# Kernel optimization log

Hardware: AMD Instinct MI355X
Metric: run time of the kernel (lower is better)

The kernel has to match this reference:

```python
import jax, jax.numpy as jnp
import numpy as np

N, D, K = 8192, 512, 256


def setup_inputs() -> dict:
    key = jax.random.key(0)
    k1, k2, k3 = jax.random.split(key, 3)
    features = jax.random.normal(k1, (N, D), dtype=jnp.float32)
    adjacency = jax.random.uniform(k2, (N, N), dtype=jnp.float32)
    W = jax.random.normal(k3, (D, K), dtype=jnp.float32) / np.sqrt(D)
    b = jnp.zeros((K,), dtype=jnp.float32)
    return {"features": features, "adjacency": adjacency, "W": W, "b": b}


def reference(features, adjacency, W, b):
    # logits = Linear(features): (n, k)
    logits = features @ W + b
    # activation == 'softmax' (torch F.softmax on 2D defaults to dim=1)
    assignments = jax.nn.softmax(logits, axis=-1)            # (n, k)
    cluster_sizes = jnp.sum(assignments, axis=0)             # (k,)
    sp = assignments / (cluster_sizes + 1e-8)                # normalized assignments (n, k)
    features_pooled = sp.T @ features                        # (k, d)
    adjacency_pooled = (sp.T @ adjacency) @ sp               # (k, k) -- computed in original forward
    # link loss: ||A - S S^T||_F / numel(A)
    diff = adjacency - sp @ sp.T                             # (n, n)
    link_loss = jnp.sqrt(jnp.sum(diff * diff)) / adjacency.size
    # entropy loss on normalized assignments
    ent_loss = jnp.mean(jnp.sum(-sp * jnp.log(sp + 1e-15), axis=-1))
    return features_pooled, assignments, adjacency_pooled, link_loss, ent_loss
```

## Files before the change

kernel.cpp:

```cpp
#include <hip/hip_runtime.h>


typedef unsigned short u16;
typedef __bf16 bf16x8 __attribute__((ext_vector_type(8)));
typedef float f32x4 __attribute__((ext_vector_type(4)));
typedef float float8_t __attribute__((ext_vector_type(8)));
typedef unsigned short ushort8_t __attribute__((ext_vector_type(8)));

#define Nn 8192
#define Dd 512
#define Kk 256

__device__ __forceinline__ u16 f2bf(float f) {
  unsigned int u = __builtin_bit_cast(unsigned int, f);
  u += 0x7FFFu + ((u >> 16) & 1u);
  return (u16)(u >> 16);
}
__device__ __forceinline__ float bf2f(u16 h) {
  return __builtin_bit_cast(float, (unsigned int)h << 16);
}
__device__ __forceinline__ void gll16(const void* g, void* l) {
  __builtin_amdgcn_global_load_lds(
      (const __attribute__((address_space(1))) unsigned int*)g,
      (__attribute__((address_space(3))) unsigned int*)l, 16, 0, 0);
}

template <bool SUMSQ, int OUTKIND, int OCC>
__launch_bounds__(256, OCC)
__global__ void gemm2(const u16* __restrict__ Apan, int ppmb,
                      const float* __restrict__ Bv, int ldb,
                      void* __restrict__ Cv, int ldc,
                      int kchunk, size_t zstride,
                      float* __restrict__ sumsq, int swz) {
  __shared__ alignas(16) u16 SH[2 * 8192 + 2 * 2048];
  float* sred = (float*)&SH[20472];

  int bx = blockIdx.x, bz = blockIdx.z;
  if (swz) {
    int gx = gridDim.x, tot = gx * gridDim.z;
    int f = bx + gx * bz;
    int l = (f & 7) * (tot >> 3) + (f >> 3);
    bx = l % gx; bz = l / gx;
  }
  const int tid = threadIdx.x, wv = tid >> 6, lane = tid & 63;
  const int l15 = lane & 15, g = lane >> 4;
  const int col0 = bx * 64;
  const int row0 = blockIdx.y * 256;
  const int kbeg = bz * kchunk;
  const int steps = kchunk >> 5;
  const u16* pbase = Apan + (size_t)(blockIdx.y * ppmb + (kbeg >> 5)) * 8192;

  float ss = 0.f;
  float8_t rb;

  auto loadB = [&](int t) {
    const int kq = kbeg + t * 32 + wv * 8;
    const float* p = Bv + (size_t)kq * ldb + col0 + lane;
#pragma unroll
    for (int i = 0; i < 8; ++i) rb[i] = p[(size_t)i * ldb];
  };
  auto storeB = [&](int buf) {
    ushort8_t h;
#pragma unroll
    for (int i = 0; i < 8; ++i) {
      h[i] = f2bf(rb[i]);
      if constexpr (SUMSQ) ss += rb[i] * rb[i];
    }
    *(uint4*)&SH[16384 + buf * 2048 + lane * 32 + wv * 8] = __builtin_bit_cast(uint4, h);
  };
  auto gllA = [&](int buf, int t) {
    const char* gp = (const char*)(pbase + (size_t)t * 8192) + wv * 4096 + lane * 16;
    char* lp = (char*)&SH[buf * 8192] + wv * 4096;
#pragma unroll
    for (int r = 0; r < 4; ++r) gll16(gp + r * 1024, lp + r * 1024);
  };

  f32x4 acc[4][4];
#pragma unroll
  for (int i = 0; i < 4; ++i)
#pragma unroll
    for (int j = 0; j < 4; ++j) acc[i][j] = (f32x4){0.f, 0.f, 0.f, 0.f};

  auto comp = [&](int buf) {
    const u16* as = &SH[buf * 8192];
    const u16* bs = &SH[16384 + buf * 2048];
    bf16x8 afr[4], bfr[4];
#pragma unroll
    for (int j = 0; j < 4; ++j)
      bfr[j] = *(const bf16x8*)(bs + (j * 16 + l15) * 32 + g * 8);
#pragma unroll
    for (int i = 0; i < 4; ++i)
      afr[i] = *(const bf16x8*)(as + (wv * 64 + i * 16 + l15) * 32 + g * 8);
#pragma unroll
    for (int i = 0; i < 4; ++i)
#pragma unroll
      for (int j = 0; j < 4; ++j)
        acc[i][j] = __builtin_amdgcn_mfma_f32_16x16x32_bf16(afr[i], bfr[j], acc[i][j], 0, 0, 0);
  };

  gllA(0, 0);
  loadB(0);
  const int last = steps - 1;

  for (int t = 0; t < steps; ++t) {
    const int cur = t & 1;
    gllA(1 - cur, (t + 1 < last) ? t + 1 : last);
    storeB(cur);
    loadB((t + 1 < last) ? t + 1 : last);
    asm volatile("s_waitcnt vmcnt(12) lgkmcnt(0)" ::: "memory");
    __builtin_amdgcn_s_barrier();
    __builtin_amdgcn_sched_barrier(0);
    comp(cur);
    __builtin_amdgcn_sched_barrier(0);
    __builtin_amdgcn_s_barrier();
  }
  asm volatile("s_waitcnt vmcnt(0) lgkmcnt(0)" ::: "memory");
  __builtin_amdgcn_s_barrier();

  if constexpr (OUTKIND == 0) {
    float* Cz = (float*)Cv + (size_t)bz * zstride;
    float* sf = (float*)SH;
#pragma unroll
    for (int h = 0; h < 2; ++h) {
      __syncthreads();
      if ((wv >> 1) == h) {
#pragma unroll
        for (int i = 0; i < 4; ++i)
#pragma unroll
          for (int j = 0; j < 4; ++j)
#pragma unroll
            for (int r = 0; r < 4; ++r)
              sf[((wv & 1) * 64 + i * 16 + g * 4 + r) * 68 + j * 16 + l15] = acc[i][j][r];
      }
      __syncthreads();
#pragma unroll
      for (int e = 0; e < 8; ++e) {
        int idx2 = tid + e * 256;
        int m = idx2 >> 4, c4 = (idx2 & 15) * 4;
        float4 v = *(const float4*)(sf + m * 68 + c4);
        *(float4*)(Cz + (size_t)(row0 + h * 128 + m) * ldc + col0 + c4) = v;
      }
    }
  } else {
    u16* C = (u16*)Cv + (size_t)bz * zstride;
    u16* sb = SH;
#pragma unroll
    for (int i = 0; i < 4; ++i)
#pragma unroll
      for (int j = 0; j < 4; ++j)
#pragma unroll
        for (int r = 0; r < 4; ++r)
          sb[(wv * 64 + i * 16 + g * 4 + r) * 72 + j * 16 + l15] = f2bf(acc[i][j][r]);
    __syncthreads();
#pragma unroll
    for (int e = 0; e < 8; ++e) {
      int m = (tid >> 3) + e * 32;
      uint4 v = *(const uint4*)(sb + m * 72 + (tid & 7) * 8);
      *(uint4*)(C + (size_t)m * ldc + col0 + (tid & 7) * 8) = v;
    }
  }

  if constexpr (SUMSQ) {
#pragma unroll
    for (int o = 32; o; o >>= 1) ss += __shfl_xor(ss, o);
    __syncthreads();
    if (lane == 0) sred[wv] = ss;
    __syncthreads();
    if (tid == 0) atomicAdd(sumsq, sred[0] + sred[1] + sred[2] + sred[3]);
  }
}

__launch_bounds__(256, 2)
__global__ void gemm1(const float* __restrict__ F, const float* __restrict__ W,
                      float* __restrict__ Cv, size_t zstride) {
  __shared__ alignas(16) u16 SH[2 * 8192 + 2 * 2048];

  const int tid = threadIdx.x, wv = tid >> 6, lane = tid & 63;
  const int l15 = lane & 15, g = lane >> 4;
  const int col0 = blockIdx.x * 64;
  const int row0 = blockIdx.y * 256;
  const int kbeg = blockIdx.z * 256;
  const int mrow = tid >> 3, kq4 = (tid & 7) * 4;

  float4 rA[8];
  float8_t rb;

  auto loadA = [&](int t) {
    const float* p = F + (size_t)(row0 + mrow) * Dd + kbeg + t * 32 + kq4;
#pragma unroll
    for (int i = 0; i < 8; ++i) rA[i] = *(const float4*)(p + (size_t)i * 32 * Dd);
  };
  auto storeA = [&](int buf) {
    u16* as = &SH[buf * 8192];
#pragma unroll
    for (int i = 0; i < 8; ++i) {
      ushort4 h = {f2bf(rA[i].x), f2bf(rA[i].y), f2bf(rA[i].z), f2bf(rA[i].w)};
      *(uint2*)(as + (mrow + i * 32) * 32 + kq4) = __builtin_bit_cast(uint2, h);
    }
  };
  auto loadB = [&](int t) {
    const int kq = kbeg + t * 32 + wv * 8;
    const float* p = W + (size_t)kq * Kk + col0 + lane;
#pragma unroll
    for (int i = 0; i < 8; ++i) rb[i] = p[(size_t)i * Kk];
  };
  auto storeB = [&](int buf) {
    ushort8_t h;
#pragma unroll
    for (int i = 0; i < 8; ++i) h[i] = f2bf(rb[i]);
    *(uint4*)&SH[16384 + buf * 2048 + lane * 32 + wv * 8] = __builtin_bit_cast(uint4, h);
  };

  f32x4 acc[4][4];
#pragma unroll
  for (int i = 0; i < 4; ++i)
#pragma unroll
    for (int j = 0; j < 4; ++j) acc[i][j] = (f32x4){0.f, 0.f, 0.f, 0.f};

  auto comp = [&](int buf) {
    const u16* as = &SH[buf * 8192];
    const u16* bs = &SH[16384 + buf * 2048];
    bf16x8 afr[4], bfr[4];
#pragma unroll
    for (int j = 0; j < 4; ++j)
      bfr[j] = *(const bf16x8*)(bs + (j * 16 + l15) * 32 + g * 8);
#pragma unroll
    for (int i = 0; i < 4; ++i)
      afr[i] = *(const bf16x8*)(as + (wv * 64 + i * 16 + l15) * 32 + g * 8);
#pragma unroll
    for (int i = 0; i < 4; ++i)
#pragma unroll
      for (int j = 0; j < 4; ++j)
        acc[i][j] = __builtin_amdgcn_mfma_f32_16x16x32_bf16(afr[i], bfr[j], acc[i][j], 0, 0, 0);
  };

  loadA(0);
  loadB(0);
  for (int t = 0; t < 8; ++t) {
    const int cur = t & 1;
    storeA(cur);
    storeB(cur);
    loadA((t + 1 < 8) ? t + 1 : 7);
    loadB((t + 1 < 8) ? t + 1 : 7);
    asm volatile("s_waitcnt vmcnt(16) lgkmcnt(0)" ::: "memory");
    __builtin_amdgcn_s_barrier();
    __builtin_amdgcn_sched_barrier(0);
    comp(cur);
    __builtin_amdgcn_sched_barrier(0);
    __builtin_amdgcn_s_barrier();
  }
  asm volatile("s_waitcnt vmcnt(0) lgkmcnt(0)" ::: "memory");
  __builtin_amdgcn_s_barrier();

  float* Cz = Cv + (size_t)blockIdx.z * zstride;
  float* sf = (float*)SH;
#pragma unroll
  for (int h = 0; h < 2; ++h) {
    __syncthreads();
    if ((wv >> 1) == h) {
#pragma unroll
      for (int i = 0; i < 4; ++i)
#pragma unroll
        for (int j = 0; j < 4; ++j)
#pragma unroll
          for (int r = 0; r < 4; ++r)
            sf[((wv & 1) * 64 + i * 16 + g * 4 + r) * 68 + j * 16 + l15] = acc[i][j][r];
    }
    __syncthreads();
#pragma unroll
    for (int e = 0; e < 8; ++e) {
      int idx2 = tid + e * 256;
      int m = idx2 >> 4, c4 = (idx2 & 15) * 4;
      float4 v = *(const float4*)(sf + m * 68 + c4);
      *(float4*)(Cz + (size_t)(row0 + h * 128 + m) * Kk + col0 + c4) = v;
    }
  }
}

__launch_bounds__(256, 2)
__global__ void gemm45(const u16* __restrict__ spTpan,
                       const float* __restrict__ F, float* __restrict__ fp_part,
                       const float* __restrict__ assign, float* __restrict__ ss_part) {
  __shared__ alignas(16) u16 SH[2 * 8192 + 2 * 2048];

  const int b = blockIdx.x;
  int bx, bz, ldb, ldc;
  const float* Bf;
  float* Cz;
  if (b < 256) {
    bx = b & 7; bz = b >> 3;
    Bf = F; ldb = Dd; ldc = Dd;
    Cz = fp_part + (size_t)bz * 131072;
  } else {
    int lb = b - 256;
    bx = lb & 3; bz = lb >> 2;
    Bf = assign; ldb = Kk; ldc = Kk;
    Cz = ss_part + (size_t)bz * 65536;
  }
  const int tid = threadIdx.x, wv = tid >> 6, lane = tid & 63;
  const int l15 = lane & 15, g = lane >> 4;
  const int col0 = bx * 64;
  const int kbeg = bz * 256;
  const u16* pbase = spTpan + (size_t)(kbeg >> 5) * 8192;

  float8_t rb;
  auto loadB = [&](int t) {
    const int kq = kbeg + t * 32 + wv * 8;
    const float* p = Bf + (size_t)kq * ldb + col0 + lane;
#pragma unroll
    for (int i = 0; i < 8; ++i) rb[i] = p[(size_t)i * ldb];
  };
  auto storeB = [&](int buf) {
    ushort8_t h;
#pragma unroll
    for (int i = 0; i < 8; ++i) h[i] = f2bf(rb[i]);
    *(uint4*)&SH[16384 + buf * 2048 + lane * 32 + wv * 8] = __builtin_bit_cast(uint4, h);
  };
  auto gllA = [&](int buf, int t) {
    const char* gp = (const char*)(pbase + (size_t)t * 8192) + wv * 4096 + lane * 16;
    char* lp = (char*)&SH[buf * 8192] + wv * 4096;
#pragma unroll
    for (int r = 0; r < 4; ++r) gll16(gp + r * 1024, lp + r * 1024);
  };

  f32x4 acc[4][4];
#pragma unroll
  for (int i = 0; i < 4; ++i)
#pragma unroll
    for (int j = 0; j < 4; ++j) acc[i][j] = (f32x4){0.f, 0.f, 0.f, 0.f};

  auto comp = [&](int buf) {
    const u16* as = &SH[buf * 8192];
    const u16* bs = &SH[16384 + buf * 2048];
    bf16x8 afr[4], bfr[4];
#pragma unroll
    for (int j = 0; j < 4; ++j)
      bfr[j] = *(const bf16x8*)(bs + (j * 16 + l15) * 32 + g * 8);
#pragma unroll
    for (int i = 0; i < 4; ++i)
      afr[i] = *(const bf16x8*)(as + (wv * 64 + i * 16 + l15) * 32 + g * 8);
#pragma unroll
    for (int i = 0; i < 4; ++i)
#pragma unroll
      for (int j = 0; j < 4; ++j)
        acc[i][j] = __builtin_amdgcn_mfma_f32_16x16x32_bf16(afr[i], bfr[j], acc[i][j], 0, 0, 0);
  };

  gllA(0, 0);
  loadB(0);
  const int last = 7;
  for (int t = 0; t < 8; ++t) {
    const int cur = t & 1;
    gllA(1 - cur, (t + 1 < last) ? t + 1 : last);
    storeB(cur);
    loadB((t + 1 < last) ? t + 1 : last);
    asm volatile("s_waitcnt vmcnt(12) lgkmcnt(0)" ::: "memory");
    __builtin_amdgcn_s_barrier();
    __builtin_amdgcn_sched_barrier(0);
    comp(cur);
    __builtin_amdgcn_sched_barrier(0);
    __builtin_amdgcn_s_barrier();
  }
  asm volatile("s_waitcnt vmcnt(0) lgkmcnt(0)" ::: "memory");
  __builtin_amdgcn_s_barrier();

  float* sf = (float*)SH;
#pragma unroll
  for (int h = 0; h < 2; ++h) {
    __syncthreads();
    if ((wv >> 1) == h) {
#pragma unroll
      for (int i = 0; i < 4; ++i)
#pragma unroll
        for (int j = 0; j < 4; ++j)
#pragma unroll
          for (int r = 0; r < 4; ++r)
            sf[((wv & 1) * 64 + i * 16 + g * 4 + r) * 68 + j * 16 + l15] = acc[i][j][r];
    }
    __syncthreads();
#pragma unroll
    for (int e = 0; e < 8; ++e) {
      int idx2 = tid + e * 256;
      int m = idx2 >> 4, c4 = (idx2 & 15) * 4;
      float4 v = *(const float4*)(sf + m * 68 + c4);
      *(float4*)(Cz + (size_t)(h * 128 + m) * ldc + col0 + c4) = v;
    }
  }
}

__launch_bounds__(256)
__global__ void softmax_rows(const float* __restrict__ lg, float* __restrict__ io,
                             const float* __restrict__ bias,
                             float* __restrict__ cs, float* __restrict__ scal) {
  if (blockIdx.x == 2048) {
    int t = threadIdx.x;
    float4 z = {0.f, 0.f, 0.f, 0.f};
    if (t < 64) ((float4*)cs)[t] = z;
    else if (t == 64) ((float4*)scal)[0] = z;
    return;
  }
  int wv = threadIdx.x >> 6, lane = threadIdx.x & 63;
  int n = blockIdx.x * 4 + wv;
  float4 b4 = ((const float4*)bias)[lane];
  float4 p0 = ((const float4*)(lg + (size_t)n * Kk))[lane];
  float4 p1 = ((const float4*)(lg + 2097152 + (size_t)n * Kk))[lane];
  float4 x = {p0.x + p1.x + b4.x, p0.y + p1.y + b4.y,
              p0.z + p1.z + b4.z, p0.w + p1.w + b4.w};
  float m = fmaxf(fmaxf(x.x, x.y), fmaxf(x.z, x.w));
#pragma unroll
  for (int o = 32; o; o >>= 1) m = fmaxf(m, __shfl_xor(m, o));
  float4 e = {__expf(x.x - m), __expf(x.y - m), __expf(x.z - m), __expf(x.w - m)};
  float s = e.x + e.y + e.z + e.w;
#pragma unroll
  for (int o = 32; o; o >>= 1) s += __shfl_xor(s, o);
  float inv = 1.f / s;
  e.x *= inv; e.y *= inv; e.z *= inv; e.w *= inv;
  ((float4*)(io + (size_t)n * Kk))[lane] = e;
}

__launch_bounds__(256)
__global__ void colsum_k(const float* __restrict__ a, float* __restrict__ cs) {
  __shared__ float4 red[4][64];
  int t = threadIdx.x, rg = t >> 6, c = t & 63;
  size_t n0 = (size_t)blockIdx.x * 128 + rg * 32;
  float4 s = {0.f, 0.f, 0.f, 0.f};
  for (int i = 0; i < 32; ++i) {
    float4 v = ((const float4*)(a + (n0 + i) * Kk))[c];
    s.x += v.x; s.y += v.y; s.z += v.z; s.w += v.w;
  }
  red[rg][c] = s;
  __syncthreads();
  if (rg == 0) {
    float4 a1 = red[1][c], a2 = red[2][c], a3 = red[3][c];
    s.x += a1.x + a2.x + a3.x; s.y += a1.y + a2.y + a3.y;
    s.z += a1.z + a2.z + a3.z; s.w += a1.w + a2.w + a3.w;
    atomicAdd(&cs[c * 4 + 0], s.x); atomicAdd(&cs[c * 4 + 1], s.y);
    atomicAdd(&cs[c * 4 + 2], s.z); atomicAdd(&cs[c * 4 + 3], s.w);
  }
}

__launch_bounds__(256)
__global__ void make_sp_pan(const float* __restrict__ a, const float* __restrict__ cs,
                            u16* __restrict__ pan, float* __restrict__ ent_sum) {
  __shared__ float sr[4];
  int p = blockIdx.x, k = threadIdx.x;
  float inv = 1.f / (cs[k] + 1e-8f);
  int n0 = p * 32;
  float ent = 0.f;
  ushort8_t h[4];
#pragma unroll
  for (int q = 0; q < 4; ++q) {
#pragma unroll
    for (int j = 0; j < 8; ++j) {
      float v = a[(size_t)(n0 + q * 8 + j) * Kk + k] * inv;
      h[q][j] = f2bf(v);
      ent -= v * __logf(v + 1e-15f);
    }
  }
  u16* dst = pan + ((size_t)p * 256 + k) * 32;
  *(uint4*)(dst + 0)  = __builtin_bit_cast(uint4, h[0]);
  *(uint4*)(dst + 8)  = __builtin_bit_cast(uint4, h[1]);
  *(uint4*)(dst + 16) = __builtin_bit_cast(uint4, h[2]);
  *(uint4*)(dst + 24) = __builtin_bit_cast(uint4, h[3]);
#pragma unroll
  for (int o = 32; o; o >>= 1) ent += __shfl_xor(ent, o);
  if ((k & 63) == 0) sr[k >> 6] = ent;
  __syncthreads();
  if (k == 0) atomicAdd(ent_sum, sr[0] + sr[1] + sr[2] + sr[3]);
}

__launch_bounds__(256)
__global__ void combine_P(const u16* __restrict__ part, u16* __restrict__ pan) {
  int idx = blockIdx.x * 256 + threadIdx.x;
  int m = idx >> 10, kk8 = idx & 1023;
  size_t off = (size_t)m * Nn + kk8 * 8;
  float8_t s = {0.f, 0.f, 0.f, 0.f, 0.f, 0.f, 0.f, 0.f};
#pragma unroll
  for (int z = 0; z < 8; ++z) {
    ushort8_t v = __builtin_bit_cast(ushort8_t,
        *(const uint4*)(part + (size_t)z * Kk * Nn + off));
#pragma unroll
    for (int j = 0; j < 8; ++j) s[j] += bf2f(v[j]);
  }
  ushort8_t h;
#pragma unroll
  for (int j = 0; j < 8; ++j) h[j] = f2bf(s[j]);
  int p = kk8 >> 2, c = (kk8 & 3) * 8;
  *(uint4*)(pan + ((size_t)p * 256 + m) * 32 + c) = __builtin_bit_cast(uint4, h);
}

__launch_bounds__(256)
__global__ void combine3(const float* __restrict__ fp_part, const float* __restrict__ ss_part,
                         const float* __restrict__ ap_part, const float* __restrict__ cs,
                         float* __restrict__ fpool, float* __restrict__ apool,
                         float* __restrict__ scal) {
  __shared__ float sr[4];
  int b = blockIdx.x, t = threadIdx.x;
  if (b < 512) {
    int i = b * 256 + t;
    float s = 0.f;
#pragma unroll
    for (int z = 0; z < 32; ++z) s += fp_part[z * 131072 + i];
    fpool[i] = s;
  } else if (b < 768) {
    int i = (b - 512) * 256 + t;
    float s = 0.f;
#pragma unroll
    for (int z = 0; z < 32; ++z) s += ss_part[z * 65536 + i];
    s *= 1.f / (cs[i & 255] + 1e-8f);
    float q = s * s;
#pragma unroll
    for (int o = 32; o; o >>= 1) q += __shfl_xor(q, o);
    if ((t & 63) == 0) sr[t >> 6] = q;
    __syncthreads();
    if (t == 0) atomicAdd(&scal[2], sr[0] + sr[1] + sr[2] + sr[3]);
  } else {
    int i = (b - 768) * 256 + t;
    float s = 0.f;
#pragma unroll
    for (int z = 0; z < 32; ++z) s += ap_part[z * 65536 + i];
    s *= 1.f / (cs[i & 255] + 1e-8f);
    apool[i] = s;
    if (i % 257 == 0) atomicAdd(&scal[3], s);
  }
}

__launch_bounds__(64)
__global__ void finalize_k(const float* __restrict__ scal,
                           float* __restrict__ olink, float* __restrict__ oent) {
  if (threadIdx.x == 0) {
    float val = scal[0] - 2.f * scal[3] + scal[2];
    *olink = sqrtf(fmaxf(val, 0.f)) / ((float)Nn * (float)Nn);
    *oent  = scal[1] / (float)Nn;
  }
}

extern "C" void kernel_launch(void* const* d_in, const int* in_sizes, int n_in,
                              void* d_out, int out_size, void* d_ws, size_t ws_size,
                              hipStream_t stream) {
  const float* F    = (const float*)d_in[0];
  const float* Adj  = (const float*)d_in[1];
  const float* W    = (const float*)d_in[2];
  const float* bias = (const float*)d_in[3];
  float* out = (float*)d_out;
  char* ws = (char*)d_ws;

  u16*  parts   = (u16*)(ws + 0);
  u16*  spTpan  = (u16*)(ws + 33554432);
  u16*  Ppan    = (u16*)(ws + 37748736);
  float* lg_part = (float*)(ws + 41943040);
  float* fp_part = (float*)(ws + 58720256);
  float* ss_part = (float*)(ws + 75497472);
  float* ap_part = (float*)(ws + 83886080);
  float* cs     = (float*)(ws + 92274688);
  float* scal   = (float*)(ws + 92275712);

  float* fpool  = out;
  float* assign = out + 131072;
  float* apool  = out + 2228224;
  float* olink  = out + 2293760;
  float* oent   = out + 2293761;

  gemm1<<<dim3(4, 32, 2), 256, 0, stream>>>(F, W, lg_part, 2097152);
  softmax_rows<<<2049, 256, 0, stream>>>(lg_part, assign, bias, cs, scal);
  colsum_k<<<64, 256, 0, stream>>>(assign, cs);
  make_sp_pan<<<256, 256, 0, stream>>>(assign, cs, spTpan, &scal[1]);

  gemm45<<<384, 256, 0, stream>>>(spTpan, F, fp_part, assign, ss_part);

  gemm2<true, 1, 4><<<dim3(128, 1, 8), 256, 0, stream>>>(
      spTpan, 256, Adj, Nn, parts, Nn, Nn / 8, (size_t)Kk * Nn, &scal[0], 1);
  combine_P<<<1024, 256, 0, stream>>>(parts, Ppan);

  gemm2<false, 0, 2><<<dim3(4, 1, 32), 256, 0, stream>>>(
      Ppan, 256, assign, Kk, ap_part, Kk, 256, 65536, nullptr, 1);

  combine3<<<1024, 256, 0, stream>>>(fp_part, ss_part, ap_part, cs, fpool, apool, scal);
  finalize_k<<<1, 64, 0, stream>>>(scal, olink, oent);
}
```

Baseline: 175.3 us.

## Add specialized adjacency GEMM with deeper register prefetch and block remapping

Replaces the generic gemm2 instantiation for the spT@Adj product with a dedicated kernel. It double-buffers the adjacency register loads (even and odd stages), so two k-steps of loads are in flight. It also raises occupancy to 3 blocks per CU and remaps block indices so neighbouring blocks share a column tile. Separately, colsum uses four times as many blocks, each summing fewer rows, to expose more parallelism. The trade-offs are more register pressure from the extra prefetch buffer and more atomics in colsum.

```diff
diff --git a/kernel.cpp b/kernel.cpp
--- a/kernel.cpp
+++ b/kernel.cpp
@@ -101,7 +101,6 @@
   gllA(0, 0);
   loadB(0);
   const int last = steps - 1;
-
   for (int t = 0; t < steps; ++t) {
     const int cur = t & 1;
     gllA(1 - cur, (t + 1 < last) ? t + 1 : last);
@@ -168,6 +167,125 @@
     __syncthreads();
     if (tid == 0) atomicAdd(sumsq, sred[0] + sred[1] + sred[2] + sred[3]);
   }
+}
+
+__launch_bounds__(256, 3)
+__global__ void gemmG2(const u16* __restrict__ spTpan,
+                       const float* __restrict__ Adj, u16* __restrict__ parts,
+                       float* __restrict__ sumsq) {
+  __shared__ alignas(16) u16 SH[2 * 8192 + 2 * 2048];
+  float* sred = (float*)&SH[20472];
+
+  int bx = blockIdx.x, bz = blockIdx.z;
+  {
+    int f = bx + 128 * bz;
+    int l = (f & 7) * 128 + (f >> 3);
+    bx = l & 127; bz = l >> 7;
+  }
+  const int tid = threadIdx.x, wv = tid >> 6, lane = tid & 63;
+  const int l15 = lane & 15, g = lane >> 4;
+  const int col0 = bx * 64;
+  const int kbeg = bz * 1024;
+  const u16* pbase = spTpan + (size_t)(kbeg >> 5) * 8192;
+
+  float ss = 0.f;
+  float8_t rbE, rbO;
+
+  auto loadB = [&](float8_t& rb, int t) {
+    const int kq = kbeg + t * 32 + wv * 8;
+    const float* p = Adj + (size_t)kq * Nn + col0 + lane;
+#pragma unroll
+    for (int i = 0; i < 8; ++i) rb[i] = p[(size_t)i * Nn];
+  };
+  auto storeB = [&](int buf, float8_t& rb) {
+    ushort8_t h;
+#pragma unroll
+    for (int i = 0; i < 8; ++i) {
+      h[i] = f2bf(rb[i]);
+      ss += rb[i] * rb[i];
+    }
+    *(uint4*)&SH[16384 + buf * 2048 + lane * 32 + wv * 8] = __builtin_bit_cast(uint4, h);
+  };
+  auto gllA = [&](int buf, int t) {
+    const char* gp = (const char*)(pbase + (size_t)t * 8192) + wv * 4096 + lane * 16;
+    char* lp = (char*)&SH[buf * 8192] + wv * 4096;
+#pragma unroll
+    for (int r = 0; r < 4; ++r) gll16(gp + r * 1024, lp + r * 1024);
+  };
+
+  f32x4 acc[4][4];
+#pragma unroll
+  for (int i = 0; i < 4; ++i)
+#pragma unroll
+    for (int j = 0; j < 4; ++j) acc[i][j] = (f32x4){0.f, 0.f, 0.f, 0.f};
+
+  auto comp = [&](int buf) {
+    const u16* as = &SH[buf * 8192];
+    const u16* bs = &SH[16384 + buf * 2048];
+    bf16x8 afr[4], bfr[4];
+#pragma unroll
+    for (int j = 0; j < 4; ++j)
+      bfr[j] = *(const bf16x8*)(bs + (j * 16 + l15) * 32 + g * 8);
+#pragma unroll
+    for (int i = 0; i < 4; ++i)
+      afr[i] = *(const bf16x8*)(as + (wv * 64 + i * 16 + l15) * 32 + g * 8);
+#pragma unroll
+    for (int i = 0; i < 4; ++i)
+#pragma unroll
+      for (int j = 0; j < 4; ++j)
+        acc[i][j] = __builtin_amdgcn_mfma_f32_16x16x32_bf16(afr[i], bfr[j], acc[i][j], 0, 0, 0);
+  };
+
+  gllA(0, 0);
+  loadB(rbE, 0);
+  loadB(rbO, 1);
+
+  for (int t = 0; t < 32; t += 2) {
+    gllA(1, (t + 1 < 31) ? t + 1 : 31);
+    storeB(0, rbE);
+    loadB(rbE, (t + 2 < 31) ? t + 2 : 31);
+    asm volatile("s_waitcnt vmcnt(20) lgkmcnt(0)" ::: "memory");
+    __builtin_amdgcn_s_barrier();
+    __builtin_amdgcn_sched_barrier(0);
+    comp(0);
+    __builtin_amdgcn_sched_barrier(0);
+    __builtin_amdgcn_s_barrier();
+    gllA(0, (t + 2 < 31) ? t + 2 : 31);
+    storeB(1, rbO);
+    loadB(rbO, (t + 3 < 31) ? t + 3 : 31);
+    asm volatile("s_waitcnt vmcnt(20) lgkmcnt(0)" ::: "memory");
+    __builtin_amdgcn_s_barrier();
+    __builtin_amdgcn_sched_barrier(0);
+    comp(1);
+    __builtin_amdgcn_sched_barrier(0);
+    __builtin_amdgcn_s_barrier();
+  }
+  asm volatile("s_waitcnt vmcnt(0) lgkmcnt(0)" ::: "memory");
+  __builtin_amdgcn_s_barrier();
+
+  u16* C = parts + (size_t)bz * ((size_t)Kk * Nn);
+  u16* sb = SH;
+#pragma unroll
+  for (int i = 0; i < 4; ++i)
+#pragma unroll
+    for (int j = 0; j < 4; ++j)
+#pragma unroll
+      for (int r = 0; r < 4; ++r)
+        sb[(wv * 64 + i * 16 + g * 4 + r) * 72 + j * 16 + l15] = f2bf(acc[i][j][r]);
+  __syncthreads();
+#pragma unroll
+  for (int e = 0; e < 8; ++e) {
+    int m = (tid >> 3) + e * 32;
+    uint4 v = *(const uint4*)(sb + m * 72 + (tid & 7) * 8);
+    *(uint4*)(C + (size_t)m * Nn + col0 + (tid & 7) * 8) = v;
+  }
+
+#pragma unroll
+  for (int o = 32; o; o >>= 1) ss += __shfl_xor(ss, o);
+  __syncthreads();
+  if (lane == 0) sred[wv] = ss;
+  __syncthreads();
+  if (tid == 0) atomicAdd(sumsq, sred[0] + sred[1] + sred[2] + sred[3]);
 }
 
 __launch_bounds__(256, 2)
@@ -422,9 +540,9 @@
 __global__ void colsum_k(const float* __restrict__ a, float* __restrict__ cs) {
   __shared__ float4 red[4][64];
   int t = threadIdx.x, rg = t >> 6, c = t & 63;
-  size_t n0 = (size_t)blockIdx.x * 128 + rg * 32;
+  size_t n0 = (size_t)blockIdx.x * 32 + rg * 8;
   float4 s = {0.f, 0.f, 0.f, 0.f};
-  for (int i = 0; i < 32; ++i) {
+  for (int i = 0; i < 8; ++i) {
     float4 v = ((const float4*)(a + (n0 + i) * Kk))[c];
     s.x += v.x; s.y += v.y; s.z += v.z; s.w += v.w;
   }
@@ -563,13 +681,12 @@
 
   gemm1<<<dim3(4, 32, 2), 256, 0, stream>>>(F, W, lg_part, 2097152);
   softmax_rows<<<2049, 256, 0, stream>>>(lg_part, assign, bias, cs, scal);
-  colsum_k<<<64, 256, 0, stream>>>(assign, cs);
+  colsum_k<<<256, 256, 0, stream>>>(assign, cs);
   make_sp_pan<<<256, 256, 0, stream>>>(assign, cs, spTpan, &scal[1]);
 
   gemm45<<<384, 256, 0, stream>>>(spTpan, F, fp_part, assign, ss_part);
 
-  gemm2<true, 1, 4><<<dim3(128, 1, 8), 256, 0, stream>>>(
-      spTpan, 256, Adj, Nn, parts, Nn, Nn / 8, (size_t)Kk * Nn, &scal[0], 1);
+  gemmG2<<<dim3(128, 1, 8), 256, 0, stream>>>(spTpan, Adj, parts, &scal[0]);
   combine_P<<<1024, 256, 0, stream>>>(parts, Ppan);
 
   gemm2<false, 0, 2><<<dim3(4, 1, 32), 256, 0, stream>>>(
```

Result: slower. 207.8 us (+18.5%).

## Fold split-K partial reduction into the second adjacency GEMM, removing combine_P

Applied to the files above, without the earlier changes.

The first adjacency GEMM now writes its eight split-K bf16 partials straight into the panel layout the MFMA kernel consumes. The second GEMM then treats the eight partials as one concatenated reduction of length 8·N, wrapping its B row index modulo N, so the separate combine_P pass and its extra buffer go away. The second GEMM runs with 64 z-slices, and combine3 sums 64 partial results. This trades one launch plus a 32MB read and 4MB write for an eightfold longer reduction in the small second GEMM. Separately, colsum_k is relaunched with more, smaller blocks.

```diff
diff --git a/kernel.cpp b/kernel.cpp
--- a/kernel.cpp
+++ b/kernel.cpp
@@ -25,7 +25,7 @@
       (__attribute__((address_space(3))) unsigned int*)l, 16, 0, 0);
 }
 
-template <bool SUMSQ, int OUTKIND, int OCC>
+template <bool SUMSQ, bool MODB, int OUTKIND, int OCC>
 __launch_bounds__(256, OCC)
 __global__ void gemm2(const u16* __restrict__ Apan, int ppmb,
                       const float* __restrict__ Bv, int ldb,
@@ -54,7 +54,8 @@
   float8_t rb;
 
   auto loadB = [&](int t) {
-    const int kq = kbeg + t * 32 + wv * 8;
+    int kq = kbeg + t * 32 + wv * 8;
+    if constexpr (MODB) kq &= (Nn - 1);
     const float* p = Bv + (size_t)kq * ldb + col0 + lane;
 #pragma unroll
     for (int i = 0; i < 8; ++i) rb[i] = p[(size_t)i * ldb];
@@ -101,7 +102,6 @@
   gllA(0, 0);
   loadB(0);
   const int last = steps - 1;
-
   for (int t = 0; t < steps; ++t) {
     const int cur = t & 1;
     gllA(1 - cur, (t + 1 < last) ? t + 1 : last);
@@ -152,11 +152,13 @@
         for (int r = 0; r < 4; ++r)
           sb[(wv * 64 + i * 16 + g * 4 + r) * 72 + j * 16 + l15] = f2bf(acc[i][j][r]);
     __syncthreads();
+    int c8 = tid & 7;
+    size_t pb = (size_t)((col0 >> 5) + (c8 >> 2)) * 8192 + (c8 & 3) * 8;
 #pragma unroll
     for (int e = 0; e < 8; ++e) {
       int m = (tid >> 3) + e * 32;
-      uint4 v = *(const uint4*)(sb + m * 72 + (tid & 7) * 8);
-      *(uint4*)(C + (size_t)m * ldc + col0 + (tid & 7) * 8) = v;
+      uint4 v = *(const uint4*)(sb + m * 72 + c8 * 8);
+      *(uint4*)(C + pb + (size_t)m * 32) = v;
     }
   }
 
@@ -422,9 +424,9 @@
 __global__ void colsum_k(const float* __restrict__ a, float* __restrict__ cs) {
   __shared__ float4 red[4][64];
   int t = threadIdx.x, rg = t >> 6, c = t & 63;
-  size_t n0 = (size_t)blockIdx.x * 128 + rg * 32;
+  size_t n0 = (size_t)blockIdx.x * 32 + rg * 8;
   float4 s = {0.f, 0.f, 0.f, 0.f};
-  for (int i = 0; i < 32; ++i) {
+  for (int i = 0; i < 8; ++i) {
     float4 v = ((const float4*)(a + (n0 + i) * Kk))[c];
     s.x += v.x; s.y += v.y; s.z += v.z; s.w += v.w;
   }
@@ -467,26 +469,6 @@
   if ((k & 63) == 0) sr[k >> 6] = ent;
   __syncthreads();
   if (k == 0) atomicAdd(ent_sum, sr[0] + sr[1] + sr[2] + sr[3]);
-}
-
-__launch_bounds__(256)
-__global__ void combine_P(const u16* __restrict__ part, u16* __restrict__ pan) {
-  int idx = blockIdx.x * 256 + threadIdx.x;
-  int m = idx >> 10, kk8 = idx & 1023;
-  size_t off = (size_t)m * Nn + kk8 * 8;
-  float8_t s = {0.f, 0.f, 0.f, 0.f, 0.f, 0.f, 0.f, 0.f};
-#pragma unroll
-  for (int z = 0; z < 8; ++z) {
-    ushort8_t v = __builtin_bit_cast(ushort8_t,
-        *(const uint4*)(part + (size_t)z * Kk * Nn + off));
-#pragma unroll
-    for (int j = 0; j < 8; ++j) s[j] += bf2f(v[j]);
-  }
-  ushort8_t h;
-#pragma unroll
-  for (int j = 0; j < 8; ++j) h[j] = f2bf(s[j]);
-  int p = kk8 >> 2, c = (kk8 & 3) * 8;
-  *(uint4*)(pan + ((size_t)p * 256 + m) * 32 + c) = __builtin_bit_cast(uint4, h);
 }
 
 __launch_bounds__(256)
@@ -518,7 +500,7 @@
     int i = (b - 768) * 256 + t;
     float s = 0.f;
 #pragma unroll
-    for (int z = 0; z < 32; ++z) s += ap_part[z * 65536 + i];
+    for (int z = 0; z < 64; ++z) s += ap_part[z * 65536 + i];
     s *= 1.f / (cs[i & 255] + 1e-8f);
     apool[i] = s;
     if (i % 257 == 0) atomicAdd(&scal[3], s);
@@ -547,13 +529,12 @@
 
   u16*  parts   = (u16*)(ws + 0);
   u16*  spTpan  = (u16*)(ws + 33554432);
-  u16*  Ppan    = (u16*)(ws + 37748736);
-  float* lg_part = (float*)(ws + 41943040);
-  float* fp_part = (float*)(ws + 58720256);
-  float* ss_part = (float*)(ws + 75497472);
-  float* ap_part = (float*)(ws + 83886080);
-  float* cs     = (float*)(ws + 92274688);
-  float* scal   = (float*)(ws + 92275712);
+  float* lg_part = (float*)(ws + 37748736);
+  float* fp_part = (float*)(ws + 54525952);
+  float* ss_part = (float*)(ws + 71303168);
+  float* ap_part = (float*)(ws + 79691776);
+  float* cs     = (float*)(ws + 96468992);
+  float* scal   = (float*)(ws + 96470016);
 
   float* fpool  = out;
   float* assign = out + 131072;
@@ -563,17 +544,16 @@
 
   gemm1<<<dim3(4, 32, 2), 256, 0, stream>>>(F, W, lg_part, 2097152);
   softmax_rows<<<2049, 256, 0, stream>>>(lg_part, assign, bias, cs, scal);
-  colsum_k<<<64, 256, 0, stream>>>(assign, cs);
+  colsum_k<<<256, 256, 0, stream>>>(assign, cs);
   make_sp_pan<<<256, 256, 0, stream>>>(assign, cs, spTpan, &scal[1]);
 
   gemm45<<<384, 256, 0, stream>>>(spTpan, F, fp_part, assign, ss_part);
 
-  gemm2<true, 1, 4><<<dim3(128, 1, 8), 256, 0, stream>>>(
-      spTpan, 256, Adj, Nn, parts, Nn, Nn / 8, (size_t)Kk * Nn, &scal[0], 1);
-  combine_P<<<1024, 256, 0, stream>>>(parts, Ppan);
-
-  gemm2<false, 0, 2><<<dim3(4, 1, 32), 256, 0, stream>>>(
-      Ppan, 256, assign, Kk, ap_part, Kk, 256, 65536, nullptr, 1);
+  gemm2<true, false, 2, 4><<<dim3(128, 1, 8), 256, 0, stream>>>(
+      spTpan, 256, Adj, Nn, parts, Nn, 1024, (size_t)Kk * Nn, &scal[0], 1);
+
+  gemm2<false, true, 0, 2><<<dim3(4, 1, 64), 256, 0, stream>>>(
+      parts, 0, assign, Kk, ap_part, Kk, 1024, 65536, nullptr, 1);
 
   combine3<<<1024, 256, 0, stream>>>(fp_part, ss_part, ap_part, cs, fpool, apool, scal);
   finalize_k<<<1, 64, 0, stream>>>(scal, olink, oent);
```

Result: slower. 224.6 us (+28.1%).
